# Kernel optimization log

Hardware: AMD Instinct MI355X
Metric: run time of the kernel (lower is better)

The kernel has to match this reference:

```python
import jax, jax.numpy as jnp
import numpy as np

B, S, HID = 1, 2048, 1024
H, HKV, D = 16, 4, 64
THETA = 10000.0


def _rope_tables(seq_len, head_dim):
    # Matches RotaryEmbedding: emb = cat(freqs, freqs); kernel reads cos/sin at even
    # positions d for each rotated pair (d, d+1), i.e. columns 0::2 of the table.
    inv_freq = 1.0 / (THETA ** (jnp.arange(0, head_dim, 2, dtype=jnp.float32) / head_dim))
    freqs = jnp.arange(seq_len, dtype=jnp.float32)[:, None] * inv_freq[None, :]  # [S, D/2]
    emb = jnp.concatenate([freqs, freqs], axis=-1)  # [S, D]
    return jnp.cos(emb)[:, 0::2], jnp.sin(emb)[:, 0::2]  # each [S, D/2]


def _apply_rope(x, cos, sin):
    # x: [B, H, S, D]; rotate interleaved pairs (2i, 2i+1) as in the kernel.
    xe, xo = x[..., 0::2], x[..., 1::2]
    re = xe * cos - xo * sin
    ro = xe * sin + xo * cos
    return jnp.stack([re, ro], axis=-1).reshape(x.shape)


def setup_inputs() -> dict:
    key = jax.random.key(0)
    k0, k1, k2, k3, k4 = jax.random.split(key, 5)
    return {
        "hidden_states": jax.random.normal(k0, (B, S, HID), dtype=jnp.float32),
        "Wq": jax.random.normal(k1, (HID, H * D), dtype=jnp.float32) * 0.02,
        "Wk": jax.random.normal(k2, (HID, HKV * D), dtype=jnp.float32) * 0.02,
        "Wv": jax.random.normal(k3, (HID, HKV * D), dtype=jnp.float32) * 0.02,
        "Wo": jax.random.normal(k4, (H * D, HID), dtype=jnp.float32) * 0.02,
    }


def reference(hidden_states, Wq, Wk, Wv, Wo):
    b, s, _ = hidden_states.shape
    q = (hidden_states @ Wq).reshape(b, s, H, D).transpose(0, 2, 1, 3)    # [B,H,S,D]
    k = (hidden_states @ Wk).reshape(b, s, HKV, D).transpose(0, 2, 1, 3)  # [B,Hkv,S,D]
    v = (hidden_states @ Wv).reshape(b, s, HKV, D).transpose(0, 2, 1, 3)

    cos, sin = _rope_tables(s, D)
    q = _apply_rope(q, cos, sin)
    k = _apply_rope(k, cos, sin)

    G = H // HKV  # GQA group size: query head h -> kv head h // G
    qg = q.reshape(b, HKV, G, s, D)
    scale = jnp.float32(D) ** -0.5
    scores = jnp.einsum("bkgqd,bkpd->bkgqp", qg, k) * scale  # [B,Hkv,G,S,S]
    causal = jnp.tril(jnp.ones((s, s), dtype=bool))
    scores = jnp.where(causal, scores, jnp.float32(-1e30))
    probs = jax.nn.softmax(scores, axis=-1)
    out = jnp.einsum("bkgqp,bkpd->bkgqd", probs, v).reshape(b, H, s, D)
    out = out.transpose(0, 2, 1, 3).reshape(b, s, H * D)
    return out @ Wo
```

## Files before the change

kernel.cpp:

```cpp
#include <hip/hip_runtime.h>
#include <hip/hip_bf16.h>
#include <math.h>

#define SEQ   2048
#define HID   1024
#define NH    16
#define NKV   4
#define DH    64
#define GQ    (NH / NKV)
#define NQKV  1536
#define LQKV  1536
#define KT    64
#define QB    32
#define CH    512
#define NCH   (SEQ / CH)
#define PSTR  72

typedef __attribute__((ext_vector_type(8))) short bf16x8;
typedef __attribute__((ext_vector_type(4))) float f32x4;
typedef unsigned short u16;
typedef unsigned int u32;

__device__ __forceinline__ u16 f2bf(float f) {
    union { float f; unsigned u; } x; x.f = f;
    unsigned r = x.u + 0x7fffu + ((x.u >> 16) & 1u);
    return (u16)(r >> 16);
}
__device__ __forceinline__ u32 pk2bf(float lo, float hi) {
    return (u32)f2bf(lo) | ((u32)f2bf(hi) << 16);
}
__device__ __forceinline__ void load_lds16(const u16* g, u16* l) {
    __builtin_amdgcn_global_load_lds(
        (const __attribute__((address_space(1))) unsigned int*)g,
        (__attribute__((address_space(3))) unsigned int*)l, 16, 0, 0);
}

__global__ __launch_bounds__(256) void prep_weights(const float* __restrict__ Wq,
                                                    const float* __restrict__ Wk,
                                                    const float* __restrict__ Wv,
                                                    const float* __restrict__ Wo,
                                                    u16* __restrict__ Wt,
                                                    u16* __restrict__ WoT) {
    const int z = blockIdx.z;
    const float* in; u16* out; int N;
    if (z == 0)      { in = Wq; out = Wt;                           N = HID; }
    else if (z == 1) { in = Wk; out = Wt + (size_t)HID * HID;       N = 256; }
    else if (z == 2) { in = Wv; out = Wt + (size_t)(HID + 256) * HID; N = 256; }
    else             { in = Wo; out = WoT;                          N = HID; }

    const int n0 = blockIdx.x * 32;
    if (n0 >= N) return;
    const int k0 = blockIdx.y * 32;

    __shared__ float t[32][33];
    const int tx = threadIdx.x & 31;
    const int ty = threadIdx.x >> 5;
    #pragma unroll
    for (int i = 0; i < 4; ++i)
        t[ty + i * 8][tx] = in[(size_t)(k0 + ty + i * 8) * N + n0 + tx];
    __syncthreads();
    #pragma unroll
    for (int i = 0; i < 4; ++i)
        out[(size_t)(n0 + ty + i * 8) * HID + k0 + tx] = f2bf(t[tx][ty + i * 8]);
}

__global__ __launch_bounds__(256) void cvt_bf16(const float* __restrict__ in,
                                                u16* __restrict__ out) {
    const int i = blockIdx.x * 256 + threadIdx.x;
    const float4 v = ((const float4*)in)[i];
    ushort4 o;
    o.x = f2bf(v.x); o.y = f2bf(v.y); o.z = f2bf(v.z); o.w = f2bf(v.w);
    ((ushort4*)out)[i] = o;
}

__global__ __launch_bounds__(256) void gemm_bt(const u16* __restrict__ A,
                                               const u16* __restrict__ Bt,
                                               float* __restrict__ C,
                                               int K, int ldc) {
    __shared__ u16 As[128 * 32];
    __shared__ u16 Bs[64 * 32];

    const int tid  = threadIdx.x;
    const int lane = tid & 63;
    const int w    = tid >> 6;
    const int m0   = blockIdx.y * 128;
    const int n0   = blockIdx.x * 64;

    const int mfrag = lane & 15;
    const int kfrag = (lane >> 4) * 8;
    const int mb    = w * 32;

    const int arow = w * 32 + (lane >> 2);
    const int acol = (lane & 3) * 8;
    const u16* gA = A  + (size_t)(m0 + arow) * K + acol;
    const u16* gB = Bt + (size_t)(n0 + w * 16 + (lane >> 2)) * K + acol;

    f32x4 acc[2][4];
    #pragma unroll
    for (int mt = 0; mt < 2; ++mt)
        #pragma unroll
        for (int nt = 0; nt < 4; ++nt)
            acc[mt][nt] = (f32x4){0.f, 0.f, 0.f, 0.f};

    for (int k0 = 0; k0 < K; k0 += 32) {
        __syncthreads();
        load_lds16(gA + k0,            &As[(w * 32) * 32]);
        load_lds16(gA + 16 * K + k0,   &As[(w * 32 + 16) * 32]);
        load_lds16(gB + k0,            &Bs[(w * 16) * 32]);
        __syncthreads();

        bf16x8 af[2], bfr[4];
        af[0] = *(const bf16x8*)&As[(mb + mfrag) * 32 + kfrag];
        af[1] = *(const bf16x8*)&As[(mb + 16 + mfrag) * 32 + kfrag];
        #pragma unroll
        for (int nt = 0; nt < 4; ++nt)
            bfr[nt] = *(const bf16x8*)&Bs[(nt * 16 + mfrag) * 32 + kfrag];

        #pragma unroll
        for (int mt = 0; mt < 2; ++mt)
            #pragma unroll
            for (int nt = 0; nt < 4; ++nt)
                acc[mt][nt] = __builtin_amdgcn_mfma_f32_16x16x32_bf16(af[mt], bfr[nt], acc[mt][nt], 0, 0, 0);
    }

    const int col   = lane & 15;
    const int rbase = (lane >> 4) * 4;
    #pragma unroll
    for (int mt = 0; mt < 2; ++mt)
        #pragma unroll
        for (int nt = 0; nt < 4; ++nt)
            #pragma unroll
            for (int rg = 0; rg < 4; ++rg)
                C[(size_t)(m0 + mb + mt * 16 + rbase + rg) * ldc + n0 + nt * 16 + col] = acc[mt][nt][rg];
}

__global__ __launch_bounds__(256) void postprocess(const float* __restrict__ QKV,
                                                   u16* __restrict__ Qb,
                                                   u16* __restrict__ Kb,
                                                   u16* __restrict__ VTg) {
    const int s   = blockIdx.x;
    const int tid = threadIdx.x;
    const float* row = QKV + (size_t)s * LQKV;
    const float ln_scale = 9.210340371976184f / 32.0f;

    #pragma unroll
    for (int it = 0; it < 2; ++it) {
        const int p = tid + it * 256;
        const int j = p & 31;
        const float inv_freq = __expf(-(float)((2 * j) & 31) * ln_scale);
        float sn, cs;
        __sincosf((float)s * inv_freq, &sn, &cs);
        const float xe = row[2 * p], xo = row[2 * p + 1];
        Qb[(size_t)s * HID + 2 * p]     = f2bf((xe * cs - xo * sn) * 0.125f);
        Qb[(size_t)s * HID + 2 * p + 1] = f2bf((xe * sn + xo * cs) * 0.125f);
    }
    if (tid < 128) {
        const int p  = tid;
        const int j  = p & 31;
        const int kh = p >> 5;
        const int d  = (2 * p) & 63;
        const float inv_freq = __expf(-(float)((2 * j) & 31) * ln_scale);
        float sn, cs;
        __sincosf((float)s * inv_freq, &sn, &cs);
        const float xe = row[1024 + 2 * p], xo = row[1024 + 2 * p + 1];
        u16* kr = Kb + ((size_t)kh * SEQ + s) * DH;
        kr[d]     = f2bf(xe * cs - xo * sn);
        kr[d + 1] = f2bf(xe * sn + xo * cs);
    }
    {
        const int c = tid;
        const int kh = c >> 6, d = c & 63;
        VTg[((size_t)kh * DH + d) * SEQ + s] = f2bf(row[1280 + c]);
    }
}

__global__ __launch_bounds__(256) void attn_kernel(const u16* __restrict__ Qb,
                                                   const u16* __restrict__ Kb,
                                                   const u16* __restrict__ VTg,
                                                   float* __restrict__ Opart,
                                                   float* __restrict__ lpart) {
    __shared__ u16 Kst[64 * PSTR];
    __shared__ u16 VTst[64 * PSTR];
    __shared__ u16 Pst[4][QB * PSTR];

    const int tid  = threadIdx.x;
    const int lane = tid & 63;
    const int w    = tid >> 6;
    const int c    = lane & 15;
    const int quad = lane >> 4;
    const int kh   = blockIdx.y;
    const int z    = blockIdx.z;
    const int qt   = (SEQ / QB - 1) - (int)blockIdx.x;
    const int q0   = qt * QB;
    const int h    = kh * GQ + w;

    const int kstart = z * CH;
    const int klim   = q0 + QB;
    if (kstart >= klim) return;
    const int kend   = (klim < kstart + CH) ? klim : (kstart + CH);
    const int ntiles = (kend - kstart + KT - 1) / KT;

    bf16x8 qf[2][2];
    #pragma unroll
    for (int g = 0; g < 2; ++g)
        #pragma unroll
        for (int ks = 0; ks < 2; ++ks)
            qf[g][ks] = *(const bf16x8*)&Qb[(size_t)(q0 + g * 16 + c) * HID + h * DH + ks * 32 + quad * 8];

    f32x4 accO[4][2];
    #pragma unroll
    for (int nt = 0; nt < 4; ++nt)
        #pragma unroll
        for (int g = 0; g < 2; ++g)
            accO[nt][g] = (f32x4){0.f, 0.f, 0.f, 0.f};
    float l[2] = {0.f, 0.f};

    for (int t = 0; t < ntiles; ++t) {
        const int kt0 = kstart + t * KT;
        __syncthreads();
        {
            const int r = tid >> 3, off = (tid & 7) * 8;
            const u16* kg = &Kb[((size_t)kh * SEQ + kt0 + r) * DH + off];
            *(uint4*)&Kst[r * PSTR + off]        = *(const uint4*)kg;
            *(uint4*)&Kst[(r + 32) * PSTR + off] = *(const uint4*)(kg + 32 * DH);
            const u16* vg = &VTg[((size_t)kh * DH + r) * SEQ + kt0 + off];
            *(uint4*)&VTst[r * PSTR + off]        = *(const uint4*)vg;
            *(uint4*)&VTst[(r + 32) * PSTR + off] = *(const uint4*)(vg + 32 * SEQ);
        }
        __syncthreads();

        f32x4 accS[4][2];
        #pragma unroll
        for (int nS = 0; nS < 4; ++nS)
            #pragma unroll
            for (int g = 0; g < 2; ++g)
                accS[nS][g] = (f32x4){0.f, 0.f, 0.f, 0.f};
        #pragma unroll
        for (int nS = 0; nS < 4; ++nS)
            #pragma unroll
            for (int ks = 0; ks < 2; ++ks) {
                const bf16x8 kf = *(const bf16x8*)&Kst[(nS * 16 + c) * PSTR + ks * 32 + quad * 8];
                #pragma unroll
                for (int g = 0; g < 2; ++g)
                    accS[nS][g] = __builtin_amdgcn_mfma_f32_16x16x32_bf16(kf, qf[g][ks], accS[nS][g], 0, 0, 0);
            }

        #pragma unroll
        for (int g = 0; g < 2; ++g) {
            const int q = q0 + g * 16 + c;
            #pragma unroll
            for (int nS = 0; nS < 4; ++nS) {
                const int key = kt0 + nS * 16 + quad * 4;
                const float p0 = (key + 0 <= q) ? __expf(accS[nS][g][0]) : 0.f;
                const float p1 = (key + 1 <= q) ? __expf(accS[nS][g][1]) : 0.f;
                const float p2 = (key + 2 <= q) ? __expf(accS[nS][g][2]) : 0.f;
                const float p3 = (key + 3 <= q) ? __expf(accS[nS][g][3]) : 0.f;
                l[g] += (p0 + p1) + (p2 + p3);
                u32* dst = (u32*)&Pst[w][(g * 16 + c) * PSTR + nS * 16 + quad * 4];
                dst[0] = pk2bf(p0, p1);
                dst[1] = pk2bf(p2, p3);
            }
        }
        __threadfence_block();

        #pragma unroll
        for (int ks2 = 0; ks2 < 2; ++ks2) {
            bf16x8 pf[2];
            #pragma unroll
            for (int g = 0; g < 2; ++g)
                pf[g] = *(const bf16x8*)&Pst[w][(g * 16 + c) * PSTR + ks2 * 32 + quad * 8];
            #pragma unroll
            for (int nt = 0; nt < 4; ++nt) {
                const bf16x8 vf = *(const bf16x8*)&VTst[(nt * 16 + c) * PSTR + ks2 * 32 + quad * 8];
                #pragma unroll
                for (int g = 0; g < 2; ++g)
                    accO[nt][g] = __builtin_amdgcn_mfma_f32_16x16x32_bf16(vf, pf[g], accO[nt][g], 0, 0, 0);
            }
        }
    }

    #pragma unroll
    for (int g = 0; g < 2; ++g) {
        float lg = l[g];
        lg += __shfl_xor(lg, 16);
        lg += __shfl_xor(lg, 32);
        if (quad == 0)
            lpart[((size_t)z * SEQ + q0 + g * 16 + c) * NH + h] = lg;

        float* Op = Opart + ((size_t)z * SEQ + q0 + g * 16 + c) * HID + h * DH;
        #pragma unroll
        for (int nt = 0; nt < 4; ++nt)
            *(f32x4*)&Op[nt * 16 + quad * 4] = accO[nt][g];
    }
}

__global__ __launch_bounds__(256) void attn_reduce(const float* __restrict__ Opart,
                                                   const float* __restrict__ lpart,
                                                   u16* __restrict__ At) {
    const int idx = blockIdx.x * 256 + threadIdx.x;
    const int q  = idx >> 8;
    const int h  = (idx & 255) >> 4;
    const int klim = (q & ~(QB - 1)) + QB;
    float4 o = ((const float4*)Opart)[idx];
    float  l = lpart[q * NH + h];
    #pragma unroll
    for (int z = 1; z < NCH; ++z) {
        if (z * CH < klim) {
            const float4 o1 = ((const float4*)Opart)[idx + z * (SEQ * HID / 4)];
            o.x += o1.x; o.y += o1.y; o.z += o1.z; o.w += o1.w;
            l += lpart[(z * SEQ + q) * NH + h];
        }
    }
    const float inv = 1.0f / l;
    ushort4 r;
    r.x = f2bf(o.x * inv); r.y = f2bf(o.y * inv);
    r.z = f2bf(o.z * inv); r.w = f2bf(o.w * inv);
    ((ushort4*)At)[idx] = r;
}

extern "C" void kernel_launch(void* const* d_in, const int* in_sizes, int n_in,
                              void* d_out, int out_size, void* d_ws, size_t ws_size,
                              hipStream_t stream) {
    const float* X  = (const float*)d_in[0];
    const float* Wq = (const float*)d_in[1];
    const float* Wk = (const float*)d_in[2];
    const float* Wv = (const float*)d_in[3];
    const float* Wo = (const float*)d_in[4];
    float* out = (float*)d_out;

    u16* Wt     = (u16*)d_ws;
    u16* WoT    = Wt + (size_t)NQKV * HID;
    u16* Xb     = WoT + (size_t)HID * HID;
    u16* At     = Xb + (size_t)SEQ * HID;
    u16* Qb     = At + (size_t)SEQ * HID;
    u16* Kb     = Qb + (size_t)SEQ * HID;
    u16* VTg    = Kb + (size_t)NKV * SEQ * DH;
    float* QKVc = (float*)(VTg + (size_t)NKV * DH * SEQ);
    float* Opart = QKVc;
    float* lpart = Opart + (size_t)NCH * SEQ * HID;

    dim3 blk(256);

    prep_weights<<<dim3(32, 32, 4), blk, 0, stream>>>(Wq, Wk, Wv, Wo, Wt, WoT);

    cvt_bf16<<<(SEQ * HID / 4) / 256, blk, 0, stream>>>(X, Xb);

    gemm_bt<<<dim3(NQKV / 64, SEQ / 128), blk, 0, stream>>>(Xb, Wt, QKVc, HID, LQKV);

    postprocess<<<SEQ, blk, 0, stream>>>(QKVc, Qb, Kb, VTg);

    attn_kernel<<<dim3(SEQ / QB, NKV, NCH), blk, 0, stream>>>(Qb, Kb, VTg, Opart, lpart);

    attn_reduce<<<(SEQ * HID / 4) / 256, blk, 0, stream>>>(Opart, lpart, At);

    gemm_bt<<<dim3(HID / 64, SEQ / 128), blk, 0, stream>>>(At, WoT, out, HID, HID);
}
```

Before: 162.2 us.

## Double-buffer B tiles and prefetch A fragments into registers in GEMM; fuse setup kernels

```diff
diff --git a/kernel.cpp b/kernel.cpp
--- a/kernel.cpp
+++ b/kernel.cpp
@@ -35,18 +35,28 @@
         (__attribute__((address_space(3))) unsigned int*)l, 16, 0, 0);
 }
 
-__global__ __launch_bounds__(256) void prep_weights(const float* __restrict__ Wq,
-                                                    const float* __restrict__ Wk,
-                                                    const float* __restrict__ Wv,
-                                                    const float* __restrict__ Wo,
-                                                    u16* __restrict__ Wt,
-                                                    u16* __restrict__ WoT) {
+__global__ __launch_bounds__(256) void setup(const float* __restrict__ X,
+                                             const float* __restrict__ Wq,
+                                             const float* __restrict__ Wk,
+                                             const float* __restrict__ Wv,
+                                             const float* __restrict__ Wo,
+                                             u16* __restrict__ Xb,
+                                             u16* __restrict__ Wt,
+                                             u16* __restrict__ WoT) {
     const int z = blockIdx.z;
+    if (z == 4) {
+        const int idx = ((int)blockIdx.y * 64 + (int)blockIdx.x) * 256 + threadIdx.x;
+        const float4 v = ((const float4*)X)[idx];
+        ushort4 o;
+        o.x = f2bf(v.x); o.y = f2bf(v.y); o.z = f2bf(v.z); o.w = f2bf(v.w);
+        ((ushort4*)Xb)[idx] = o;
+        return;
+    }
     const float* in; u16* out; int N;
-    if (z == 0)      { in = Wq; out = Wt;                           N = HID; }
-    else if (z == 1) { in = Wk; out = Wt + (size_t)HID * HID;       N = 256; }
+    if (z == 0)      { in = Wq; out = Wt;                             N = HID; }
+    else if (z == 1) { in = Wk; out = Wt + (size_t)HID * HID;         N = 256; }
     else if (z == 2) { in = Wv; out = Wt + (size_t)(HID + 256) * HID; N = 256; }
-    else             { in = Wo; out = WoT;                          N = HID; }
+    else             { in = Wo; out = WoT;                            N = HID; }
 
     const int n0 = blockIdx.x * 32;
     if (n0 >= N) return;
@@ -64,36 +74,27 @@
         out[(size_t)(n0 + ty + i * 8) * HID + k0 + tx] = f2bf(t[tx][ty + i * 8]);
 }
 
-__global__ __launch_bounds__(256) void cvt_bf16(const float* __restrict__ in,
-                                                u16* __restrict__ out) {
-    const int i = blockIdx.x * 256 + threadIdx.x;
-    const float4 v = ((const float4*)in)[i];
-    ushort4 o;
-    o.x = f2bf(v.x); o.y = f2bf(v.y); o.z = f2bf(v.z); o.w = f2bf(v.w);
-    ((ushort4*)out)[i] = o;
-}
-
-__global__ __launch_bounds__(256) void gemm_bt(const u16* __restrict__ A,
+__global__ __launch_bounds__(256) void gemm_v2(const u16* __restrict__ A,
                                                const u16* __restrict__ Bt,
                                                float* __restrict__ C,
                                                int K, int ldc) {
-    __shared__ u16 As[128 * 32];
-    __shared__ u16 Bs[64 * 32];
+    __shared__ u16 Bs[2][64 * 32];
 
     const int tid  = threadIdx.x;
     const int lane = tid & 63;
     const int w    = tid >> 6;
+    const int c    = lane & 15;
+    const int quad = lane >> 4;
     const int m0   = blockIdx.y * 128;
     const int n0   = blockIdx.x * 64;
 
-    const int mfrag = lane & 15;
-    const int kfrag = (lane >> 4) * 8;
-    const int mb    = w * 32;
-
-    const int arow = w * 32 + (lane >> 2);
-    const int acol = (lane & 3) * 8;
-    const u16* gA = A  + (size_t)(m0 + arow) * K + acol;
-    const u16* gB = Bt + (size_t)(n0 + w * 16 + (lane >> 2)) * K + acol;
+    const u16* gB  = Bt + (size_t)(n0 + w * 16 + (lane >> 2)) * K + (lane & 3) * 8;
+    u16* const bdst = (u16*)&Bs[0][0] + (w * 16) * 32;
+
+    const u16* gA0 = A + (size_t)(m0 + w * 32 + c) * K + quad * 8;
+    const u16* gA1 = gA0 + (size_t)16 * K;
+
+    const int T = K / 32;
 
     f32x4 acc[2][4];
     #pragma unroll
@@ -102,36 +103,38 @@
         for (int nt = 0; nt < 4; ++nt)
             acc[mt][nt] = (f32x4){0.f, 0.f, 0.f, 0.f};
 
-    for (int k0 = 0; k0 < K; k0 += 32) {
+    bf16x8 afc[2], afn[2];
+    afc[0] = *(const bf16x8*)gA0;
+    afc[1] = *(const bf16x8*)gA1;
+    load_lds16(gB, bdst);
+
+    for (int t = 0; t < T; ++t) {
         __syncthreads();
-        load_lds16(gA + k0,            &As[(w * 32) * 32]);
-        load_lds16(gA + 16 * K + k0,   &As[(w * 32 + 16) * 32]);
-        load_lds16(gB + k0,            &Bs[(w * 16) * 32]);
-        __syncthreads();
-
-        bf16x8 af[2], bfr[4];
-        af[0] = *(const bf16x8*)&As[(mb + mfrag) * 32 + kfrag];
-        af[1] = *(const bf16x8*)&As[(mb + 16 + mfrag) * 32 + kfrag];
+        if (t + 1 < T) {
+            load_lds16(gB + (t + 1) * 32, bdst + ((t + 1) & 1) * (64 * 32));
+            afn[0] = *(const bf16x8*)(gA0 + (t + 1) * 32);
+            afn[1] = *(const bf16x8*)(gA1 + (t + 1) * 32);
+        }
+        bf16x8 bfr[4];
         #pragma unroll
         for (int nt = 0; nt < 4; ++nt)
-            bfr[nt] = *(const bf16x8*)&Bs[(nt * 16 + mfrag) * 32 + kfrag];
-
+            bfr[nt] = *(const bf16x8*)&Bs[t & 1][(nt * 16 + c) * 32 + quad * 8];
         #pragma unroll
         for (int mt = 0; mt < 2; ++mt)
             #pragma unroll
             for (int nt = 0; nt < 4; ++nt)
-                acc[mt][nt] = __builtin_amdgcn_mfma_f32_16x16x32_bf16(af[mt], bfr[nt], acc[mt][nt], 0, 0, 0);
-    }
-
-    const int col   = lane & 15;
-    const int rbase = (lane >> 4) * 4;
+                acc[mt][nt] = __builtin_amdgcn_mfma_f32_16x16x32_bf16(afc[mt], bfr[nt], acc[mt][nt], 0, 0, 0);
+        afc[0] = afn[0];
+        afc[1] = afn[1];
+    }
+
     #pragma unroll
     for (int mt = 0; mt < 2; ++mt)
         #pragma unroll
         for (int nt = 0; nt < 4; ++nt)
             #pragma unroll
             for (int rg = 0; rg < 4; ++rg)
-                C[(size_t)(m0 + mb + mt * 16 + rbase + rg) * ldc + n0 + nt * 16 + col] = acc[mt][nt][rg];
+                C[(size_t)(m0 + w * 32 + mt * 16 + quad * 4 + rg) * ldc + n0 + nt * 16 + c] = acc[mt][nt][rg];
 }
 
 __global__ __launch_bounds__(256) void postprocess(const float* __restrict__ QKV,
@@ -341,11 +344,9 @@
 
     dim3 blk(256);
 
-    prep_weights<<<dim3(32, 32, 4), blk, 0, stream>>>(Wq, Wk, Wv, Wo, Wt, WoT);
-
-    cvt_bf16<<<(SEQ * HID / 4) / 256, blk, 0, stream>>>(X, Xb);
-
-    gemm_bt<<<dim3(NQKV / 64, SEQ / 128), blk, 0, stream>>>(Xb, Wt, QKVc, HID, LQKV);
+    setup<<<dim3(64, 32, 5), blk, 0, stream>>>(X, Wq, Wk, Wv, Wo, Xb, Wt, WoT);
+
+    gemm_v2<<<dim3(NQKV / 64, SEQ / 128), blk, 0, stream>>>(Xb, Wt, QKVc, HID, LQKV);
 
     postprocess<<<SEQ, blk, 0, stream>>>(QKVc, Qb, Kb, VTg);
 
@@ -353,5 +354,5 @@
 
     attn_reduce<<<(SEQ * HID / 4) / 256, blk, 0, stream>>>(Opart, lpart, At);
 
-    gemm_bt<<<dim3(HID / 64, SEQ / 128), blk, 0, stream>>>(At, WoT, out, HID, HID);
-}
+    gemm_v2<<<dim3(HID / 64, SEQ / 128), blk, 0, stream>>>(At, WoT, out, HID, HID);
+}
```

Result: faster. 158.6 us (-2.2%).
